# Kernel tuning notes

Measured on AMD Instinct MI355X. Metric: run time of the kernel, lower is better.

The kernel has to match this reference:

```python
import jax, jax.numpy as jnp
import numpy as np
from jax import lax

D_MODEL = 512
N_BLOCKS = 8
VOCAB = 2048
MEL = 80
D_INNER = 2 * D_MODEL      # standard Mamba expand=2
STATE = 16                 # AudioConstants.MAMBA_STATE_DIM
DT_RANK = D_MODEL // 16    # 32
CONV_K = 4                 # causal depthwise conv kernel
B, T = 4, 2048


def setup_inputs() -> dict:
    key = jax.random.key(0)
    ks = jax.random.split(key, 16)
    s = 0.02
    nb = N_BLOCKS
    inp = {
        "feats": jax.random.normal(ks[0], (B, T, MEL), jnp.float32),
        "feat_lens": jax.random.randint(ks[1], (B,), 0, T, jnp.int32),
        # frontend
        "conv1_w": jax.random.normal(ks[2], (D_MODEL, MEL, 3), jnp.float32) * s,
        "conv1_b": jnp.zeros((D_MODEL,), jnp.float32),
        "conv2_w": jax.random.normal(ks[3], (D_MODEL, D_MODEL, 3), jnp.float32) * s,
        "conv2_b": jnp.zeros((D_MODEL,), jnp.float32),
        # stacked per-block Mamba params (leading dim = n_blocks)
        "norm_w": jnp.ones((nb, D_MODEL), jnp.float32),
        "in_proj_w": jax.random.normal(ks[4], (nb, D_MODEL, 2 * D_INNER), jnp.float32) * s,
        "dwconv_w": jax.random.normal(ks[5], (nb, D_INNER, CONV_K), jnp.float32) * s,
        "dwconv_b": jnp.zeros((nb, D_INNER), jnp.float32),
        "x_proj_w": jax.random.normal(ks[6], (nb, D_INNER, DT_RANK + 2 * STATE), jnp.float32) * s,
        "dt_proj_w": jax.random.normal(ks[7], (nb, DT_RANK, D_INNER), jnp.float32) * s,
        "dt_proj_b": jnp.full((nb, D_INNER), -4.6, jnp.float32),  # softplus(-4.6)~0.01
        "A_log": jnp.tile(jnp.log(jnp.arange(1, STATE + 1, dtype=jnp.float32))[None, None, :], (nb, D_INNER, 1)),
        "Dskip": jnp.ones((nb, D_INNER), jnp.float32),
        "out_proj_w": jax.random.normal(ks[8], (nb, D_INNER, D_MODEL), jnp.float32) * s,
        # CTC head
        "head_w": jax.random.normal(ks[9], (D_MODEL, VOCAB), jnp.float32) * s,
        "head_b": jnp.zeros((VOCAB,), jnp.float32),
    }
    return inp


def _conv1d(x, w, b, stride, pad):
    # x: (B, Cin, L), w: (Cout, Cin, K)
    y = lax.conv_general_dilated(x, w, (stride,), [(pad, pad)],
                                 dimension_numbers=("NCH", "OIH", "NCH"))
    return y + b[None, :, None]


def _mamba_layer(x, p):
    nw, ipw, cw, cb, xpw, dpw, dpb, alog, dsk, opw = p
    res = x
    # RMSNorm
    xn = x * lax.rsqrt(jnp.mean(x * x, axis=-1, keepdims=True) + 1e-5) * nw
    xz = xn @ ipw                                # (B, L, 2*di)
    xs, z = jnp.split(xz, 2, axis=-1)
    # causal depthwise conv over time
    xc = jnp.pad(xs.transpose(0, 2, 1), ((0, 0), (0, 0), (CONV_K - 1, 0)))
    xc = lax.conv_general_dilated(xc, cw[:, None, :], (1,), [(0, 0)],
                                  dimension_numbers=("NCH", "OIH", "NCH"),
                                  feature_group_count=D_INNER)
    xs = jax.nn.silu((xc + cb[None, :, None]).transpose(0, 2, 1))  # (B, L, di)
    # input-dependent SSM params
    xdb = xs @ xpw                               # (B, L, dt_rank + 2N)
    dt, Bm, Cm = jnp.split(xdb, [DT_RANK, DT_RANK + STATE], axis=-1)
    delta = jax.nn.softplus(dt @ dpw + dpb)      # (B, L, di)
    A = -jnp.exp(alog)                           # (di, N)
    dA = jnp.exp(delta[..., None] * A)           # (B, L, di, N)
    dBx = delta[..., None] * Bm[:, :, None, :] * xs[..., None]

    def step(h, inp):
        dA_t, dBx_t, C_t = inp                   # (B,di,N),(B,di,N),(B,N)
        h = dA_t * h + dBx_t
        y = jnp.einsum("bdn,bn->bd", h, C_t)
        return h, y

    h0 = jnp.zeros((x.shape[0], D_INNER, STATE), x.dtype)
    _, ys = lax.scan(step, h0, (dA.transpose(1, 0, 2, 3),
                                dBx.transpose(1, 0, 2, 3),
                                Cm.transpose(1, 0, 2)))
    y = ys.transpose(1, 0, 2) + xs * dsk          # (B, L, di)
    y = y * jax.nn.silu(z)
    return res + y @ opw, None


def reference(feats, feat_lens, conv1_w, conv1_b, conv2_w, conv2_b,
              norm_w, in_proj_w, dwconv_w, dwconv_b, x_proj_w,
              dt_proj_w, dt_proj_b, A_log, Dskip, out_proj_w,
              head_w, head_b):
    x = feats.transpose(0, 2, 1)                  # (B, 80, T)
    x = jax.nn.gelu(_conv1d(x, conv1_w, conv1_b, 2, 1), approximate=False)
    x = jax.nn.gelu(_conv1d(x, conv2_w, conv2_b, 2, 1), approximate=False)
    x = x.transpose(0, 2, 1)                      # (B, T/4, D)
    params = (norm_w, in_proj_w, dwconv_w, dwconv_b, x_proj_w,
              dt_proj_w, dt_proj_b, A_log, Dskip, out_proj_w)
    x, _ = lax.scan(_mamba_layer, x, params)
    logits = x @ head_w + head_b                  # (B, T/4, V)
    out_lens = jnp.maximum(feat_lens // 4, 1)
    return logits, out_lens
```

## Files before the change

### kernel.cpp

```cpp
#include <hip/hip_runtime.h>
#include <hip/hip_bf16.h>

#define DMODEL 512
#define NB 8
#define VOCABSZ 2048
#define MEL 80
#define DIN 1024
#define NSTATE 16
#define BATCH 4
#define TIN 2048
#define LL1 1024
#define LSEQ 512
#define MROWS (BATCH*LSEQ)
#define M1ROWS (BATCH*LL1)
#define NCHUNK 16
#define LCHUNK 32

typedef unsigned short u16;
typedef unsigned int   u32;
typedef __attribute__((ext_vector_type(8))) short short8;
typedef __attribute__((ext_vector_type(4))) float f32x4;

__device__ __forceinline__ float bf2f(u16 v) { return __uint_as_float(((u32)v) << 16); }
__device__ __forceinline__ u16 f2bf(float f) {
    u32 u = __float_as_uint(f);
    return (u16)((u + 0x7fffu + ((u >> 16) & 1u)) >> 16);
}
__device__ __forceinline__ float gelu_exact(float v) {
    return 0.5f * v * (1.0f + erff(v * 0.70710678118654752f));
}
__device__ __forceinline__ float silu_f(float v) { return v / (1.0f + __expf(-v)); }
__device__ __forceinline__ float softplus_f(float v) { return v > 20.f ? v : log1pf(__expf(v)); }

template<int WM, int WN, int MR, int NR, int EPI, int SPLITK>
__global__ __launch_bounds__(WM*WN*64) void gemm3_bf16(
    const u16* __restrict__ A, int lda,
    const u16* __restrict__ BT, int ldb,
    const float* __restrict__ bias,
    float* __restrict__ Cf, u16* __restrict__ Cb, int ldc,
    int K, int zstride)
{
    constexpr int BM = WM * MR * 16;
    constexpr int BN = WN * NR * 16;
    constexpr int NT = WM * WN * 64;
    constexpr int LA = (BM * 4) / NT;
    constexpr int LB = (BN * 4) / NT;
    __shared__ __align__(16) u16 As[2][2 * BM * 32];
    __shared__ __align__(16) u16 Bs[2][2 * BN * 32];
    __shared__ float s_sc[EPI == 7 ? BM : 1];
    const int tid = threadIdx.x;
    const int m0 = blockIdx.y * BM, n0 = blockIdx.x * BN;
    const int lane = tid & 63;
    const int wave = tid >> 6;
    const int wm = wave / WN, wn = wave % WN;
    const int lr = lane & 15, lk = lane >> 4;

    int kt0 = 0, kend = K;
    if (SPLITK > 1) {
        const int kb = K / SPLITK;
        kt0 = blockIdx.z * kb;
        kend = kt0 + kb;
        Cf += (size_t)blockIdx.z * zstride;
    }

    f32x4 acc[MR][NR];
#pragma unroll
    for (int m = 0; m < MR; ++m)
#pragma unroll
        for (int n = 0; n < NR; ++n) acc[m][n] = (f32x4){0.f, 0.f, 0.f, 0.f};
    float ssq[MR];
#pragma unroll
    for (int m = 0; m < MR; ++m) ssq[m] = 0.f;

    auto stage = [&](int buf, int kt) {
#pragma unroll
        for (int h = 0; h < 2; ++h) {
#pragma unroll
            for (int c = 0; c < LA; ++c) {
                int idx = c * NT + tid;
                const u16* src = A + (size_t)(m0 + (idx >> 2)) * lda + kt + h * 32 + (idx & 3) * 8;
                __builtin_amdgcn_global_load_lds(
                    (const __attribute__((address_space(1))) void*)src,
                    (__attribute__((address_space(3))) void*)&As[buf][h * BM * 32 + idx * 8], 16, 0, 0);
            }
#pragma unroll
            for (int c = 0; c < LB; ++c) {
                int idx = c * NT + tid;
                const u16* src = BT + (size_t)(n0 + (idx >> 2)) * ldb + kt + h * 32 + (idx & 3) * 8;
                __builtin_amdgcn_global_load_lds(
                    (const __attribute__((address_space(1))) void*)src,
                    (__attribute__((address_space(3))) void*)&Bs[buf][h * BN * 32 + idx * 8], 16, 0, 0);
            }
        }
    };

    stage(0, kt0);
    __syncthreads();
    int cur = 0;
    for (int kt = kt0; kt < kend; kt += 64) {
        if (kt + 64 < kend) stage(cur ^ 1, kt + 64);
        short8 a0[MR], a1[MR], b0[NR], b1[NR];
#pragma unroll
        for (int m = 0; m < MR; ++m) {
            a0[m] = *(const short8*)&As[cur][((wm * MR + m) * 16 + lr) * 32 + lk * 8];
            a1[m] = *(const short8*)&As[cur][BM * 32 + ((wm * MR + m) * 16 + lr) * 32 + lk * 8];
        }
#pragma unroll
        for (int n = 0; n < NR; ++n) {
            b0[n] = *(const short8*)&Bs[cur][((wn * NR + n) * 16 + lr) * 32 + lk * 8];
            b1[n] = *(const short8*)&Bs[cur][BN * 32 + ((wn * NR + n) * 16 + lr) * 32 + lk * 8];
        }
        if (EPI == 7 && wn == 0) {
#pragma unroll
            for (int m = 0; m < MR; ++m)
#pragma unroll
                for (int j = 0; j < 8; ++j) {
                    float v0 = bf2f((u16)a0[m][j]);
                    float v1 = bf2f((u16)a1[m][j]);
                    ssq[m] = fmaf(v0, v0, ssq[m]);
                    ssq[m] = fmaf(v1, v1, ssq[m]);
                }
        }
#pragma unroll
        for (int m = 0; m < MR; ++m)
#pragma unroll
            for (int n = 0; n < NR; ++n) {
                acc[m][n] = __builtin_amdgcn_mfma_f32_16x16x32_bf16(a0[m], b0[n], acc[m][n], 0, 0, 0);
                acc[m][n] = __builtin_amdgcn_mfma_f32_16x16x32_bf16(a1[m], b1[n], acc[m][n], 0, 0, 0);
            }
        __syncthreads();
        cur ^= 1;
    }

    if (EPI == 7) {
        if (wn == 0) {
#pragma unroll
            for (int m = 0; m < MR; ++m) {
                float ss = ssq[m];
                ss += __shfl_xor(ss, 16);
                ss += __shfl_xor(ss, 32);
                if (lk == 0)
                    s_sc[(wm * MR + m) * 16 + lr] = rsqrtf(ss * (1.f / 512.f) + 1e-5f);
            }
        }
        __syncthreads();
    }

#pragma unroll
    for (int m = 0; m < MR; ++m) {
#pragma unroll
        for (int n = 0; n < NR; ++n) {
#pragma unroll
            for (int r = 0; r < 4; ++r) {
                const int lrow = (wm * MR + m) * 16 + lk * 4 + r;
                const int row = m0 + lrow;
                const int col = n0 + (wn * NR + n) * 16 + lr;
                float v = acc[m][n][r];
                if (EPI == 1)      v += bias[col];
                else if (EPI == 2) v = gelu_exact(v + bias[col]);
                else if (EPI == 3) v = softplus_f(v + bias[col]);
                else if (EPI == 4) v += Cf[(size_t)row * ldc + col];
                else if (EPI == 7) v *= s_sc[lrow];
                if (Cf) Cf[(size_t)row * ldc + col] = v;
                if (Cb) Cb[(size_t)row * ldc + col] = f2bf(v);
            }
        }
    }
}

__global__ __launch_bounds__(256) void tcast_k(const float* __restrict__ in, u16* __restrict__ out,
                                               int R, int C, size_t sin, size_t sout) {
    in  += (size_t)blockIdx.z * sin;
    out += (size_t)blockIdx.z * sout;
    __shared__ float s[32][33];
    const int tx = threadIdx.x & 31, ty = threadIdx.x >> 5;
    const int r0 = blockIdx.y * 32, c0 = blockIdx.x * 32;
#pragma unroll
    for (int i = 0; i < 4; ++i)
        s[ty + i * 8][tx] = in[(size_t)(r0 + ty + i * 8) * C + c0 + tx];
    __syncthreads();
#pragma unroll
    for (int i = 0; i < 4; ++i)
        out[(size_t)(c0 + ty + i * 8) * R + r0 + tx] = f2bf(s[tx][ty + i * 8]);
}

__global__ __launch_bounds__(256) void tcast_nw_k(const float* __restrict__ in, u16* __restrict__ out,
                                                  const float* __restrict__ nwp,
                                                  int R, int C, size_t sin, size_t sout, int nws) {
    in  += (size_t)blockIdx.z * sin;
    out += (size_t)blockIdx.z * sout;
    nwp += (size_t)blockIdx.z * nws;
    __shared__ float s[32][33];
    const int tx = threadIdx.x & 31, ty = threadIdx.x >> 5;
    const int r0 = blockIdx.y * 32, c0 = blockIdx.x * 32;
#pragma unroll
    for (int i = 0; i < 4; ++i)
        s[ty + i * 8][tx] = in[(size_t)(r0 + ty + i * 8) * C + c0 + tx];
    __syncthreads();
    const float nwv = nwp[r0 + tx];
#pragma unroll
    for (int i = 0; i < 4; ++i)
        out[(size_t)(c0 + ty + i * 8) * R + r0 + tx] = f2bf(s[tx][ty + i * 8] * nwv);
}

__global__ void castpad_k(const float* __restrict__ in, u16* __restrict__ out,
                          int rows, int cin, int cout, int instride,
                          size_t sin, size_t sout) {
    in  += (size_t)blockIdx.z * sin;
    out += (size_t)blockIdx.z * sout;
    int idx = blockIdx.x * 256 + threadIdx.x;
    if (idx >= rows * cout) return;
    int c = idx % cout, r = idx / cout;
    out[idx] = (c < cin) ? f2bf(in[(size_t)r * instride + c]) : (u16)0;
}

__global__ void im2col1_k(const float* __restrict__ feats, u16* __restrict__ out,
                          const int* __restrict__ feat_lens, float* __restrict__ lens_out) {
    int idx = blockIdx.x * 256 + threadIdx.x;
    if (blockIdx.x == 0 && threadIdx.x < BATCH) {
        int v = feat_lens[threadIdx.x] / 4;
        if (v < 1) v = 1;
        lens_out[threadIdx.x] = (float)v;
    }
    int c = idx & 255, m = idx >> 8;
    int l1 = m & (LL1 - 1), b = m >> 10;
    float v = 0.f;
    if (c < 240) {
        int ci = c / 3, kk = c - ci * 3;
        int t = 2 * l1 - 1 + kk;
        if (t >= 0 && t < TIN) v = feats[((size_t)b * TIN + t) * MEL + ci];
    }
    out[idx] = f2bf(v);
}

__global__ void im2col2_k(const u16* __restrict__ y1b, u16* __restrict__ out) {
    int idx = blockIdx.x * 256 + threadIdx.x;
    int c = idx % 1536, m = idx / 1536;
    int l = m & (LSEQ - 1), b = m >> 9;
    int ci = c / 3, kk = c - ci * 3;
    int t = 2 * l - 1 + kk;
    out[idx] = (t >= 0 && t < LL1) ? y1b[((size_t)b * LL1 + t) * 512 + ci] : (u16)0;
}

__global__ __launch_bounds__(256) void dwconv_silu_k(const u16* __restrict__ xzb,
                                                     const float* __restrict__ cw,
                                                     const float* __restrict__ cb,
                                                     u16* __restrict__ xsb) {
    int d = blockIdx.x * 256 + threadIdx.x;
    int m = blockIdx.y;
    int l = m & (LSEQ - 1);
    int b = m >> 9;
    float acc = cb[d];
    const float4 w4 = *reinterpret_cast<const float4*>(&cw[d * 4]);
    const float wk[4] = {w4.x, w4.y, w4.z, w4.w};
#pragma unroll
    for (int k = 0; k < 4; k++) {
        int t = l - 3 + k;
        if (t >= 0) acc += wk[k] * bf2f(xzb[((size_t)(b * LSEQ + t)) * (2 * DIN) + d]);
    }
    xsb[(size_t)m * DIN + d] = f2bf(silu_f(acc));
}

__global__ __launch_bounds__(256) void dtproj_k(
    const float* __restrict__ part, const u16* __restrict__ dpwT,
    const float* __restrict__ dpb, u16* __restrict__ delb)
{
    __shared__ __align__(16) u16 As[128 * 32];
    __shared__ __align__(16) u16 Bs[64 * 32];
    const int tid = threadIdx.x;
    const int m0 = blockIdx.y * 128, n0 = blockIdx.x * 64;
    {
        const int r = tid >> 1, hh = (tid & 1) * 16;
        const size_t o = (size_t)(m0 + r) * 64 + hh;
        float4 s[4];
#pragma unroll
        for (int q = 0; q < 4; ++q) {
            s[q] = *(const float4*)&part[o + q * 4];
#pragma unroll
            for (int p = 1; p < 4; ++p) {
                const float4 v = *(const float4*)&part[(size_t)p * 131072 + o + q * 4];
                s[q].x += v.x; s[q].y += v.y; s[q].z += v.z; s[q].w += v.w;
            }
        }
        u32 pk[8];
#pragma unroll
        for (int q = 0; q < 4; ++q) {
            pk[2 * q]     = (u32)f2bf(s[q].x) | ((u32)f2bf(s[q].y) << 16);
            pk[2 * q + 1] = (u32)f2bf(s[q].z) | ((u32)f2bf(s[q].w) << 16);
        }
        *(uint4*)&As[r * 32 + hh]     = make_uint4(pk[0], pk[1], pk[2], pk[3]);
        *(uint4*)&As[r * 32 + hh + 8] = make_uint4(pk[4], pk[5], pk[6], pk[7]);
    }
    {
        const int row = tid >> 2, p4 = (tid & 3) * 8;
        const u16* src = dpwT + (size_t)(n0 + row) * 32 + p4;
        __builtin_amdgcn_global_load_lds(
            (const __attribute__((address_space(1))) void*)src,
            (__attribute__((address_space(3))) void*)&Bs[row * 32 + p4], 16, 0, 0);
    }
    __syncthreads();
    const int lane = tid & 63, wave = tid >> 6;
    const int wm = wave >> 1, wn = wave & 1;
    const int lr = lane & 15, lk = lane >> 4;
    short8 b8[2];
#pragma unroll
    for (int n = 0; n < 2; ++n)
        b8[n] = *(const short8*)&Bs[((wn * 2 + n) * 16 + lr) * 32 + lk * 8];
#pragma unroll
    for (int m = 0; m < 4; ++m) {
        const short8 a8 = *(const short8*)&As[((wm * 4 + m) * 16 + lr) * 32 + lk * 8];
#pragma unroll
        for (int n = 0; n < 2; ++n) {
            f32x4 acc = __builtin_amdgcn_mfma_f32_16x16x32_bf16(a8, b8[n], (f32x4){0.f,0.f,0.f,0.f}, 0, 0, 0);
#pragma unroll
            for (int r = 0; r < 4; ++r) {
                const int row = m0 + (wm * 4 + m) * 16 + lk * 4 + r;
                const int col = n0 + (wn * 2 + n) * 16 + lr;
                delb[(size_t)row * DIN + col] = f2bf(softplus_f(acc[r] + dpb[col]));
            }
        }
    }
}

template<int PASS>
__global__ __launch_bounds__(256) void scan_chunk_k(
    const u16* __restrict__ deltab, const u16* __restrict__ xsb,
    const float* __restrict__ part, const u16* __restrict__ xzb,
    const float* __restrict__ alog, const float* __restrict__ dsk,
    float* __restrict__ P, float* __restrict__ Q,
    u16* __restrict__ yb)
{
    __shared__ float s_bc[LCHUNK * 32];
    __shared__ float s_dl[LCHUNK * 64];
    __shared__ float s_xs[LCHUNK * 64];
    __shared__ float s_z [PASS ? LCHUNK * 64 : 1];

    const int tid  = threadIdx.x;
    const int j    = tid & 3;
    const int dsub = tid >> 2;
    const int d0   = blockIdx.x * 64;
    const int c    = blockIdx.y;
    const int b    = blockIdx.z;
    const int d    = d0 + dsub;
    const size_t rbase = (size_t)b * LSEQ + c * LCHUNK;

    for (int idx = tid; idx < LCHUNK * 32; idx += 256) {
        int t = idx >> 5, cc = idx & 31;
        const size_t o = (rbase + t) * 64 + 32 + cc;
        s_bc[idx] = part[o] + part[131072 + o] + part[262144 + o] + part[393216 + o];
    }
    for (int idx = tid; idx < LCHUNK * 64; idx += 256) {
        int t = idx >> 6, dd = idx & 63;
        s_dl[idx] = bf2f(deltab[(rbase + t) * DIN + d0 + dd]);
        s_xs[idx] = bf2f(xsb[(rbase + t) * DIN + d0 + dd]);
        if (PASS) s_z[idx] = bf2f(xzb[(rbase + t) * (2 * DIN) + DIN + d0 + dd]);
    }
    __syncthreads();

    float a[4], h[4];
#pragma unroll
    for (int nj = 0; nj < 4; nj++)
        a[nj] = -__expf(alog[(size_t)d * NSTATE + j * 4 + nj]);

    const size_t chstride = (size_t)DIN * NSTATE;
    const size_t chcol = (size_t)d * NSTATE + j * 4;
    h[0] = h[1] = h[2] = h[3] = 0.f;
    if (PASS) {
        for (int c2 = 0; c2 < c; ++c2) {
            const size_t o = ((size_t)(b * NCHUNK + c2)) * chstride + chcol;
            const float4 Pv = *(const float4*)&P[o];
            const float4 Qv = *(const float4*)&Q[o];
            h[0] = fmaf(Pv.x, h[0], Qv.x);
            h[1] = fmaf(Pv.y, h[1], Qv.y);
            h[2] = fmaf(Pv.z, h[2], Qv.z);
            h[3] = fmaf(Pv.w, h[3], Qv.w);
        }
    }
    const float dskv = PASS ? dsk[d] : 0.f;
    float sdl = 0.f;

    for (int t = 0; t < LCHUNK; t++) {
        const float dl = s_dl[t * 64 + dsub];
        const float xv = s_xs[t * 64 + dsub];
        const float dlx = dl * xv;
        if (!PASS) sdl += dl;
        float yv = 0.f;
#pragma unroll
        for (int nj = 0; nj < 4; nj++) {
            const float bn = s_bc[t * 32 + j * 4 + nj];
            const float dA = __expf(dl * a[nj]);
            h[nj] = fmaf(dA, h[nj], dlx * bn);
            if (PASS) {
                const float cn = s_bc[t * 32 + 16 + j * 4 + nj];
                yv = fmaf(h[nj], cn, yv);
            }
        }
        if (PASS) {
            yv += __shfl_xor(yv, 1);
            yv += __shfl_xor(yv, 2);
            if (j == 0) {
                const float zv = s_z[t * 64 + dsub];
                yb[(rbase + t) * DIN + d] = f2bf((yv + xv * dskv) * silu_f(zv));
            }
        }
    }

    if (!PASS) {
        const size_t o = ((size_t)(b * NCHUNK + c)) * chstride + chcol;
        float4 Pv, Qv;
        Pv.x = __expf(a[0] * sdl); Pv.y = __expf(a[1] * sdl);
        Pv.z = __expf(a[2] * sdl); Pv.w = __expf(a[3] * sdl);
        Qv.x = h[0]; Qv.y = h[1]; Qv.z = h[2]; Qv.w = h[3];
        *(float4*)&P[o] = Pv;
        *(float4*)&Q[o] = Qv;
    }
}

extern "C" void kernel_launch(void* const* d_in, const int* in_sizes, int n_in,
                              void* d_out, int out_size, void* d_ws, size_t ws_size,
                              hipStream_t stream)
{
    const float* feats = (const float*)d_in[0];
    const int*   flens = (const int*)  d_in[1];
    const float* c1w = (const float*)d_in[2];
    const float* c1b = (const float*)d_in[3];
    const float* c2w = (const float*)d_in[4];
    const float* c2b = (const float*)d_in[5];
    const float* nw  = (const float*)d_in[6];
    const float* ipw = (const float*)d_in[7];
    const float* cw  = (const float*)d_in[8];
    const float* cb  = (const float*)d_in[9];
    const float* xpw = (const float*)d_in[10];
    const float* dpw = (const float*)d_in[11];
    const float* dpb = (const float*)d_in[12];
    const float* alog= (const float*)d_in[13];
    const float* dskp= (const float*)d_in[14];
    const float* opw = (const float*)d_in[15];
    const float* hw  = (const float*)d_in[16];
    const float* hb  = (const float*)d_in[17];

    float* ws = (float*)d_ws;
    u16*  XZb    = (u16*)ws;
    float* X     = ws + 2097152;
    u16*  Xb     = (u16*)(ws + 3145728);
    u16*  XSb    = (u16*)(ws + 4194304);
    u16*  DELb   = (u16*)(ws + 5242880);
    float* P     = ws + 6291456;
    u16*  Yb     = (u16*)(ws + 7340032);
    float* XDBp  = ws + 8388608;
    u16*  ipwTa  = (u16*)(ws + 10125312);
    u16*  opwTa  = (u16*)(ws + 14319616);
    u16*  hwT    = (u16*)(ws + 16416768);
    u16*  xpwT   = (u16*)(ws + 16941056);
    u16*  dpwT   = (u16*)(ws + 17203200);
    u16*  c1wb   = (u16*)(ws + 17334272);
    u16*  c2wb   = (u16*)(ws + 17399808);
    u16*  Y1b    = XSb;
    float* logits = (float*)d_out;
    float* Q     = logits;

    castpad_k<<<dim3(512, 1, 1), 256, 0, stream>>>(c1w, c1wb, 512, 240, 256, 240, 0, 0);
    castpad_k<<<dim3(3072, 1, 1), 256, 0, stream>>>(c2w, c2wb, 512, 1536, 1536, 1536, 0, 0);
    tcast_k<<<dim3(64, 16, 1), 256, 0, stream>>>(hw, hwT, 512, 2048, 0, 0);
    tcast_k<<<dim3(2, 32, 8), 256, 0, stream>>>(xpw, xpwT, 1024, 64, 65536, 65536);
    tcast_k<<<dim3(32, 1, 8), 256, 0, stream>>>(dpw, dpwT, 32, 1024, 32768, 32768);
    tcast_nw_k<<<dim3(64, 16, 8), 256, 0, stream>>>(ipw, ipwTa, nw, 512, 2048,
                                                    1048576, 1048576, DMODEL);
    tcast_k<<<dim3(16, 32, 8), 256, 0, stream>>>(opw, opwTa, 1024, 512, 524288, 524288);

    im2col1_k<<<4096, 256, 0, stream>>>(feats, XZb, flens, logits + (size_t)MROWS * VOCABSZ);
    gemm3_bf16<2, 2, 4, 2, 2, 1><<<dim3(8, 32), 256, 0, stream>>>(
        XZb, 256, c1wb, 256, c1b, nullptr, Y1b, 512, 256, 0);
    im2col2_k<<<12288, 256, 0, stream>>>(Y1b, XZb);
    gemm3_bf16<2, 2, 2, 2, 2, 1><<<dim3(8, 32), 256, 0, stream>>>(
        XZb, 1536, c2wb, 1536, c2b, X, Xb, 512, 1536, 0);

    for (int blk = 0; blk < NB; ++blk) {
        gemm3_bf16<2, 2, 4, 2, 7, 1><<<dim3(32, 16), 256, 0, stream>>>(
            Xb, 512, ipwTa + (size_t)blk * 1048576, 512, nullptr,
            nullptr, XZb, 2048, 512, 0);
        dwconv_silu_k<<<dim3(4, MROWS), 256, 0, stream>>>(
            XZb, cw + blk * DIN * 4, cb + blk * DIN, XSb);
        gemm3_bf16<2, 2, 2, 2, 0, 4><<<dim3(1, 32, 4), 256, 0, stream>>>(
            XSb, 1024, xpwT + (size_t)blk * 65536, 1024, nullptr,
            XDBp, nullptr, 64, 1024, 131072);
        dtproj_k<<<dim3(16, 16), 256, 0, stream>>>(
            XDBp, dpwT + (size_t)blk * 32768, dpb + blk * DIN, DELb);
        scan_chunk_k<0><<<dim3(16, NCHUNK, BATCH), 256, 0, stream>>>(
            DELb, XSb, XDBp, nullptr, alog + (size_t)blk * DIN * NSTATE,
            nullptr, P, Q, nullptr);
        scan_chunk_k<1><<<dim3(16, NCHUNK, BATCH), 256, 0, stream>>>(
            DELb, XSb, XDBp, XZb, alog + (size_t)blk * DIN * NSTATE,
            dskp + blk * DIN, P, Q, Yb);
        gemm3_bf16<2, 2, 2, 2, 4, 1><<<dim3(8, 32), 256, 0, stream>>>(
            Yb, 1024, opwTa + (size_t)blk * 524288, 1024, nullptr,
            X, Xb, 512, 1024, 0);
    }

    gemm3_bf16<2, 2, 4, 2, 1, 1><<<dim3(32, 16), 256, 0, stream>>>(
        Xb, 512, hwT, 512, hb, logits, nullptr, 2048, 512, 0);
}
```

Baseline: 822.2 us.

## Fuse dt projection into scan kernels and merge weight-prep launches

Removes the separate dtproj MFMA kernel and recomputes the delta projection plus softplus inside both scan passes, from the dt partial sums and transposed dt weights, in FP32 FMA. This drops one launch per block and the DELb bf16 round-trip through global memory. Both scan passes now redo the 32-wide dot product per element. The seven weight-cast and transpose launches are also merged into one prep_k kernel to cut launch overhead.

```diff
diff --git a/kernel.cpp b/kernel.cpp
--- a/kernel.cpp
+++ b/kernel.cpp
@@ -158,7 +158,6 @@
                 float v = acc[m][n][r];
                 if (EPI == 1)      v += bias[col];
                 else if (EPI == 2) v = gelu_exact(v + bias[col]);
-                else if (EPI == 3) v = softplus_f(v + bias[col]);
                 else if (EPI == 4) v += Cf[(size_t)row * ldc + col];
                 else if (EPI == 7) v *= s_sc[lrow];
                 if (Cf) Cf[(size_t)row * ldc + col] = v;
@@ -168,50 +167,70 @@
     }
 }
 
-__global__ __launch_bounds__(256) void tcast_k(const float* __restrict__ in, u16* __restrict__ out,
-                                               int R, int C, size_t sin, size_t sout) {
-    in  += (size_t)blockIdx.z * sin;
-    out += (size_t)blockIdx.z * sout;
-    __shared__ float s[32][33];
+__device__ __forceinline__ void tp_tile(float (*s)[33], const float* __restrict__ in,
+                                        u16* __restrict__ out, int R, int C, int tile,
+                                        const float* __restrict__ nwp) {
     const int tx = threadIdx.x & 31, ty = threadIdx.x >> 5;
-    const int r0 = blockIdx.y * 32, c0 = blockIdx.x * 32;
+    const int tC = C / 32;
+    const int r0 = (tile / tC) * 32, c0 = (tile % tC) * 32;
 #pragma unroll
     for (int i = 0; i < 4; ++i)
         s[ty + i * 8][tx] = in[(size_t)(r0 + ty + i * 8) * C + c0 + tx];
     __syncthreads();
-#pragma unroll
-    for (int i = 0; i < 4; ++i)
-        out[(size_t)(c0 + ty + i * 8) * R + r0 + tx] = f2bf(s[tx][ty + i * 8]);
-}
-
-__global__ __launch_bounds__(256) void tcast_nw_k(const float* __restrict__ in, u16* __restrict__ out,
-                                                  const float* __restrict__ nwp,
-                                                  int R, int C, size_t sin, size_t sout, int nws) {
-    in  += (size_t)blockIdx.z * sin;
-    out += (size_t)blockIdx.z * sout;
-    nwp += (size_t)blockIdx.z * nws;
-    __shared__ float s[32][33];
-    const int tx = threadIdx.x & 31, ty = threadIdx.x >> 5;
-    const int r0 = blockIdx.y * 32, c0 = blockIdx.x * 32;
-#pragma unroll
-    for (int i = 0; i < 4; ++i)
-        s[ty + i * 8][tx] = in[(size_t)(r0 + ty + i * 8) * C + c0 + tx];
-    __syncthreads();
-    const float nwv = nwp[r0 + tx];
+    const float nwv = nwp ? nwp[r0 + tx] : 1.f;
 #pragma unroll
     for (int i = 0; i < 4; ++i)
         out[(size_t)(c0 + ty + i * 8) * R + r0 + tx] = f2bf(s[tx][ty + i * 8] * nwv);
 }
 
-__global__ void castpad_k(const float* __restrict__ in, u16* __restrict__ out,
-                          int rows, int cin, int cout, int instride,
-                          size_t sin, size_t sout) {
-    in  += (size_t)blockIdx.z * sin;
-    out += (size_t)blockIdx.z * sout;
-    int idx = blockIdx.x * 256 + threadIdx.x;
-    if (idx >= rows * cout) return;
-    int c = idx % cout, r = idx / cout;
-    out[idx] = (c < cin) ? f2bf(in[(size_t)r * instride + c]) : (u16)0;
+__global__ __launch_bounds__(256) void prep_k(
+    const float* __restrict__ hw, u16* __restrict__ hwT,
+    const float* __restrict__ xpw, u16* __restrict__ xpwT,
+    const float* __restrict__ dpw, u16* __restrict__ dpwT,
+    const float* __restrict__ ipw, u16* __restrict__ ipwTa, const float* __restrict__ nw,
+    const float* __restrict__ opw, u16* __restrict__ opwTa,
+    const float* __restrict__ c1w, u16* __restrict__ c1wb,
+    const float* __restrict__ c2w, u16* __restrict__ c2wb)
+{
+    __shared__ float s[32][33];
+    int id = blockIdx.x;
+    if (id < 1024) { tp_tile(s, hw, hwT, 512, 2048, id, nullptr); return; }
+    id -= 1024;
+    if (id < 512) {
+        int z = id >> 6, t = id & 63;
+        tp_tile(s, xpw + (size_t)z * 65536, xpwT + (size_t)z * 65536, 1024, 64, t, nullptr);
+        return;
+    }
+    id -= 512;
+    if (id < 256) {
+        int z = id >> 5, t = id & 31;
+        tp_tile(s, dpw + (size_t)z * 32768, dpwT + (size_t)z * 32768, 32, 1024, t, nullptr);
+        return;
+    }
+    id -= 256;
+    if (id < 8192) {
+        int z = id >> 10, t = id & 1023;
+        tp_tile(s, ipw + (size_t)z * 1048576, ipwTa + (size_t)z * 1048576, 512, 2048, t, nw + z * DMODEL);
+        return;
+    }
+    id -= 8192;
+    if (id < 4096) {
+        int z = id >> 9, t = id & 511;
+        tp_tile(s, opw + (size_t)z * 524288, opwTa + (size_t)z * 524288, 1024, 512, t, nullptr);
+        return;
+    }
+    id -= 4096;
+    if (id < 512) {
+        int idx = id * 256 + threadIdx.x;
+        int c = idx & 255, r = idx >> 8;
+        c1wb[idx] = (c < 240) ? f2bf(c1w[r * 240 + c]) : (u16)0;
+        return;
+    }
+    id -= 512;
+    {
+        int idx = id * 256 + threadIdx.x;
+        c2wb[idx] = f2bf(c2w[idx]);
+    }
 }
 
 __global__ void im2col1_k(const float* __restrict__ feats, u16* __restrict__ out,
@@ -261,76 +280,17 @@
     xsb[(size_t)m * DIN + d] = f2bf(silu_f(acc));
 }
 
-__global__ __launch_bounds__(256) void dtproj_k(
-    const float* __restrict__ part, const u16* __restrict__ dpwT,
-    const float* __restrict__ dpb, u16* __restrict__ delb)
-{
-    __shared__ __align__(16) u16 As[128 * 32];
-    __shared__ __align__(16) u16 Bs[64 * 32];
-    const int tid = threadIdx.x;
-    const int m0 = blockIdx.y * 128, n0 = blockIdx.x * 64;
-    {
-        const int r = tid >> 1, hh = (tid & 1) * 16;
-        const size_t o = (size_t)(m0 + r) * 64 + hh;
-        float4 s[4];
-#pragma unroll
-        for (int q = 0; q < 4; ++q) {
-            s[q] = *(const float4*)&part[o + q * 4];
-#pragma unroll
-            for (int p = 1; p < 4; ++p) {
-                const float4 v = *(const float4*)&part[(size_t)p * 131072 + o + q * 4];
-                s[q].x += v.x; s[q].y += v.y; s[q].z += v.z; s[q].w += v.w;
-            }
-        }
-        u32 pk[8];
-#pragma unroll
-        for (int q = 0; q < 4; ++q) {
-            pk[2 * q]     = (u32)f2bf(s[q].x) | ((u32)f2bf(s[q].y) << 16);
-            pk[2 * q + 1] = (u32)f2bf(s[q].z) | ((u32)f2bf(s[q].w) << 16);
-        }
-        *(uint4*)&As[r * 32 + hh]     = make_uint4(pk[0], pk[1], pk[2], pk[3]);
-        *(uint4*)&As[r * 32 + hh + 8] = make_uint4(pk[4], pk[5], pk[6], pk[7]);
-    }
-    {
-        const int row = tid >> 2, p4 = (tid & 3) * 8;
-        const u16* src = dpwT + (size_t)(n0 + row) * 32 + p4;
-        __builtin_amdgcn_global_load_lds(
-            (const __attribute__((address_space(1))) void*)src,
-            (__attribute__((address_space(3))) void*)&Bs[row * 32 + p4], 16, 0, 0);
-    }
-    __syncthreads();
-    const int lane = tid & 63, wave = tid >> 6;
-    const int wm = wave >> 1, wn = wave & 1;
-    const int lr = lane & 15, lk = lane >> 4;
-    short8 b8[2];
-#pragma unroll
-    for (int n = 0; n < 2; ++n)
-        b8[n] = *(const short8*)&Bs[((wn * 2 + n) * 16 + lr) * 32 + lk * 8];
-#pragma unroll
-    for (int m = 0; m < 4; ++m) {
-        const short8 a8 = *(const short8*)&As[((wm * 4 + m) * 16 + lr) * 32 + lk * 8];
-#pragma unroll
-        for (int n = 0; n < 2; ++n) {
-            f32x4 acc = __builtin_amdgcn_mfma_f32_16x16x32_bf16(a8, b8[n], (f32x4){0.f,0.f,0.f,0.f}, 0, 0, 0);
-#pragma unroll
-            for (int r = 0; r < 4; ++r) {
-                const int row = m0 + (wm * 4 + m) * 16 + lk * 4 + r;
-                const int col = n0 + (wn * 2 + n) * 16 + lr;
-                delb[(size_t)row * DIN + col] = f2bf(softplus_f(acc[r] + dpb[col]));
-            }
-        }
-    }
-}
-
 template<int PASS>
 __global__ __launch_bounds__(256) void scan_chunk_k(
-    const u16* __restrict__ deltab, const u16* __restrict__ xsb,
-    const float* __restrict__ part, const u16* __restrict__ xzb,
+    const u16* __restrict__ xsb, const float* __restrict__ part,
+    const u16* __restrict__ xzb,
+    const u16* __restrict__ dpwT, const float* __restrict__ dpb,
     const float* __restrict__ alog, const float* __restrict__ dsk,
     float* __restrict__ P, float* __restrict__ Q,
     u16* __restrict__ yb)
 {
     __shared__ float s_bc[LCHUNK * 32];
+    __shared__ float s_dt[LCHUNK * 32];
     __shared__ float s_dl[LCHUNK * 64];
     __shared__ float s_xs[LCHUNK * 64];
     __shared__ float s_z [PASS ? LCHUNK * 64 : 1];
@@ -346,14 +306,47 @@
 
     for (int idx = tid; idx < LCHUNK * 32; idx += 256) {
         int t = idx >> 5, cc = idx & 31;
-        const size_t o = (rbase + t) * 64 + 32 + cc;
-        s_bc[idx] = part[o] + part[131072 + o] + part[262144 + o] + part[393216 + o];
+        const size_t o = (rbase + t) * 64 + cc;
+        s_dt[idx] = part[o] + part[131072 + o] + part[262144 + o] + part[393216 + o];
+        const size_t o2 = o + 32;
+        s_bc[idx] = part[o2] + part[131072 + o2] + part[262144 + o2] + part[393216 + o2];
     }
     for (int idx = tid; idx < LCHUNK * 64; idx += 256) {
         int t = idx >> 6, dd = idx & 63;
-        s_dl[idx] = bf2f(deltab[(rbase + t) * DIN + d0 + dd]);
         s_xs[idx] = bf2f(xsb[(rbase + t) * DIN + d0 + dd]);
         if (PASS) s_z[idx] = bf2f(xzb[(rbase + t) * (2 * DIN) + DIN + d0 + dd]);
+    }
+    __syncthreads();
+
+    {
+        const int dd = tid & 63, tq = tid >> 6;
+        const u16* wrow = dpwT + (size_t)(d0 + dd) * 32;
+        const uint4 w0 = *(const uint4*)&wrow[0];
+        const uint4 w1 = *(const uint4*)&wrow[8];
+        const uint4 w2 = *(const uint4*)&wrow[16];
+        const uint4 w3 = *(const uint4*)&wrow[24];
+        const u32 wa[16] = {w0.x, w0.y, w0.z, w0.w, w1.x, w1.y, w1.z, w1.w,
+                            w2.x, w2.y, w2.z, w2.w, w3.x, w3.y, w3.z, w3.w};
+        float wk[32];
+#pragma unroll
+        for (int k = 0; k < 16; ++k) {
+            wk[2 * k]     = bf2f((u16)(wa[k] & 0xffffu));
+            wk[2 * k + 1] = bf2f((u16)(wa[k] >> 16));
+        }
+        const float bias = dpb[d0 + dd];
+        float accv[8];
+#pragma unroll
+        for (int tt = 0; tt < 8; ++tt) accv[tt] = bias;
+#pragma unroll
+        for (int k = 0; k < 32; ++k) {
+            const float w = wk[k];
+#pragma unroll
+            for (int tt = 0; tt < 8; ++tt)
+                accv[tt] = fmaf(s_dt[(tq * 8 + tt) * 32 + k], w, accv[tt]);
+        }
+#pragma unroll
+        for (int tt = 0; tt < 8; ++tt)
+            s_dl[(tq * 8 + tt) * 64 + dd] = softplus_f(accv[tt]);
     }
     __syncthreads();
 
@@ -444,7 +437,6 @@
     float* X     = ws + 2097152;
     u16*  Xb     = (u16*)(ws + 3145728);
     u16*  XSb    = (u16*)(ws + 4194304);
-    u16*  DELb   = (u16*)(ws + 5242880);
     float* P     = ws + 6291456;
     u16*  Yb     = (u16*)(ws + 7340032);
     float* XDBp  = ws + 8388608;
@@ -459,14 +451,9 @@
     float* logits = (float*)d_out;
     float* Q     = logits;
 
-    castpad_k<<<dim3(512, 1, 1), 256, 0, stream>>>(c1w, c1wb, 512, 240, 256, 240, 0, 0);
-    castpad_k<<<dim3(3072, 1, 1), 256, 0, stream>>>(c2w, c2wb, 512, 1536, 1536, 1536, 0, 0);
-    tcast_k<<<dim3(64, 16, 1), 256, 0, stream>>>(hw, hwT, 512, 2048, 0, 0);
-    tcast_k<<<dim3(2, 32, 8), 256, 0, stream>>>(xpw, xpwT, 1024, 64, 65536, 65536);
-    tcast_k<<<dim3(32, 1, 8), 256, 0, stream>>>(dpw, dpwT, 32, 1024, 32768, 32768);
-    tcast_nw_k<<<dim3(64, 16, 8), 256, 0, stream>>>(ipw, ipwTa, nw, 512, 2048,
-                                                    1048576, 1048576, DMODEL);
-    tcast_k<<<dim3(16, 32, 8), 256, 0, stream>>>(opw, opwTa, 1024, 512, 524288, 524288);
+    prep_k<<<17664, 256, 0, stream>>>(hw, hwT, xpw, xpwT, dpw, dpwT,
+                                      ipw, ipwTa, nw, opw, opwTa,
+                                      c1w, c1wb, c2w, c2wb);
 
     im2col1_k<<<4096, 256, 0, stream>>>(feats, XZb, flens, logits + (size_t)MROWS * VOCABSZ);
     gemm3_bf16<2, 2, 4, 2, 2, 1><<<dim3(8, 32), 256, 0, stream>>>(
@@ -484,14 +471,12 @@
         gemm3_bf16<2, 2, 2, 2, 0, 4><<<dim3(1, 32, 4), 256, 0, stream>>>(
             XSb, 1024, xpwT + (size_t)blk * 65536, 1024, nullptr,
             XDBp, nullptr, 64, 1024, 131072);
-        dtproj_k<<<dim3(16, 16), 256, 0, stream>>>(
-            XDBp, dpwT + (size_t)blk * 32768, dpb + blk * DIN, DELb);
         scan_chunk_k<0><<<dim3(16, NCHUNK, BATCH), 256, 0, stream>>>(
-            DELb, XSb, XDBp, nullptr, alog + (size_t)blk * DIN * NSTATE,
-            nullptr, P, Q, nullptr);
+            XSb, XDBp, nullptr, dpwT + (size_t)blk * 32768, dpb + blk * DIN,
+            alog + (size_t)blk * DIN * NSTATE, nullptr, P, Q, nullptr);
         scan_chunk_k<1><<<dim3(16, NCHUNK, BATCH), 256, 0, stream>>>(
-            DELb, XSb, XDBp, XZb, alog + (size_t)blk * DIN * NSTATE,
-            dskp + blk * DIN, P, Q, Yb);
+            XSb, XDBp, XZb, dpwT + (size_t)blk * 32768, dpb + blk * DIN,
+            alog + (size_t)blk * DIN * NSTATE, dskp + blk * DIN, P, Q, Yb);
         gemm3_bf16<2, 2, 2, 2, 4, 1><<<dim3(8, 32), 256, 0, stream>>>(
             Yb, 1024, opwTa + (size_t)blk * 524288, 1024, nullptr,
             X, Xb, 512, 1024, 0);
```

Result: slower. 1.264 ms (+53.7%).
